# Performance work log

Hardware: AMD Instinct MI355X
Metric: run time of the kernel (lower is better)

## Reference

```python
import jax, jax.numpy as jnp
import numpy as np

LN_EPS = 1e-5   # torch nn.LayerNorm default eps
L2_EPS = 1e-12  # torch F.normalize default eps


def setup_inputs() -> dict:
    key = jax.random.key(0)
    k1, k2 = jax.random.split(key)
    b, c, h, w = 4, 256, 128, 256
    num_classes, num_prototype, proj_dim = 19, 10, 256
    x = jax.random.normal(k1, (b, c, h, w), dtype=jnp.float32)
    # trunc_normal_(std=0.02) approximated by normal * 0.02 (l2-normalized in fwd anyway)
    prototypes = jax.random.normal(k2, (num_classes, num_prototype, proj_dim), dtype=jnp.float32) * 0.02
    mask_norm_weight = jnp.ones((num_classes,), dtype=jnp.float32)
    mask_norm_bias = jnp.zeros((num_classes,), dtype=jnp.float32)
    return {"x": x, "prototypes": prototypes,
            "mask_norm_weight": mask_norm_weight, "mask_norm_bias": mask_norm_bias}


def _layer_norm(y, w, b):
    mu = jnp.mean(y, axis=-1, keepdims=True)
    var = jnp.var(y, axis=-1, keepdims=True)
    return (y - mu) * jax.lax.rsqrt(var + LN_EPS) * w + b


def reference(x, prototypes, mask_norm_weight, mask_norm_bias):
    b, c, h, w = x.shape
    # self.prototypes.data.copy_(l2_normalize(self.prototypes)) -- normalize over feature dim
    protos = prototypes / (jnp.linalg.norm(prototypes, axis=-1, keepdims=True) + L2_EPS)
    # rearrange 'b c h w -> (b h w) c'
    xf = x.transpose(0, 2, 3, 1).reshape(-1, c)           # [n, d]
    # cosine similarity: einsum('nd,kmd->nmk') then permute -> [n, k(classes), m(protos)]
    sim_mat = jnp.einsum('nd,kmd->nkm', xf, protos)       # [n, cls, proto]
    out_seg = jnp.max(sim_mat, axis=2)                    # amax over prototypes -> [n, cls]
    out_seg = _layer_norm(out_seg, mask_norm_weight, mask_norm_bias)
    # rearrange '(b h w) c -> b c h w'
    return out_seg.reshape(b, h, w, -1).transpose(0, 3, 1, 2)
```

## Files before the change

kernel.cpp:

```cpp
#include <hip/hip_runtime.h>


#define CC_   256
#define HW_   32768
#define NPIX_ 131072
#define NCLS_ 19
#define NPROT_ 10
#define NT_   12
#define MBLK_ 128
#define NCHUNK_ 8
#define ABUF_  16384
#define BBUF_  24576

typedef __attribute__((ext_vector_type(8))) short bf16x8;
typedef __attribute__((ext_vector_type(4))) float f32x4;

__device__ __forceinline__ void gll16(const void* g, void* l) {
  __builtin_amdgcn_global_load_lds((__attribute__((address_space(1))) void*)(g),
                                   (__attribute__((address_space(3))) void*)(l), 16, 0, 0);
}

__global__ void prep_protos(const float* __restrict__ protos, char* __restrict__ Bp) {
  const int p = blockIdx.x;
  const int l = threadIdx.x;
  __shared__ float pn[256];
  float v[4] = {0.f, 0.f, 0.f, 0.f};
  float sq = 0.f;
  if (p < 190) {
    #pragma unroll
    for (int i = 0; i < 4; ++i) {
      v[i] = protos[p * 256 + l * 4 + i];
      sq += v[i] * v[i];
    }
  }
  #pragma unroll
  for (int off = 32; off > 0; off >>= 1) sq += __shfl_xor(sq, off, 64);
  const float scale = (p < 190) ? 1.0f / (sqrtf(sq) + 1e-12f) : 0.0f;
  #pragma unroll
  for (int i = 0; i < 4; ++i) pn[l * 4 + i] = v[i] * scale;
  __syncthreads();

  const int oct  = l >> 1;
  const int part = l & 1;
  bf16x8 o8;
  #pragma unroll
  for (int i = 0; i < 8; ++i) {
    const float f = pn[oct * 8 + i];
    const unsigned bits = __builtin_bit_cast(unsigned, f);
    if (part == 0) {
      o8[i] = (short)(bits >> 16);
    } else {
      const float hf = __builtin_bit_cast(float, bits & 0xFFFF0000u);
      const float lf = f - hf;
      o8[i] = (short)(__builtin_bit_cast(unsigned, lf) >> 16);
    }
  }
  const int cc = oct >> 2, oL = oct & 3;
  const int nt = p >> 4;
  const int j2 = nt * 2 + part;
  const int lane = (oL << 4) | (p & 15);
  *(bf16x8*)(Bp + (size_t)(((cc * 24 + j2) * 64 + lane) * 16)) = o8;
}

__device__ __forceinline__ void convert_write(char* Adst, const float* xv,
                                              int chalf, int mt, int r15) {
  #pragma unroll
  for (int o2 = 0; o2 < 2; ++o2) {
    const int oct = chalf * 2 + o2;
    bf16x8 h, l;
    #pragma unroll
    for (int i = 0; i < 8; ++i) {
      const float f = xv[o2 * 8 + i];
      const unsigned bits = __builtin_bit_cast(unsigned, f);
      const float hf = __builtin_bit_cast(float, bits & 0xFFFF0000u);
      const float lf = f - hf;
      h[i] = (short)(bits >> 16);
      l[i] = (short)(__builtin_bit_cast(unsigned, lf) >> 16);
    }
    *(bf16x8*)(Adst + ((0 * 8 + mt) * 64 + (oct << 4) + r15) * 16) = h;
    *(bf16x8*)(Adst + ((1 * 8 + mt) * 64 + (oct << 4) + r15) * 16) = l;
  }
}

__launch_bounds__(256, 2)
__global__ void gemm_kernel(const float* __restrict__ x, const char* __restrict__ Bp,
                            const float* __restrict__ mw, const float* __restrict__ mb,
                            float* __restrict__ out) {
  __shared__ __align__(16) char smem[81920];
  char* Abase = smem;
  char* Bbase = smem + 32768;

  const int tid  = threadIdx.x;
  const int wave = tid >> 6;
  const int lane = tid & 63;
  const int n0   = blockIdx.x * MBLK_;
  const int b    = n0 >> 15;
  const int hw0  = n0 & (HW_ - 1);
  const float* xb = x + (size_t)b * CC_ * HW_ + hw0;

  const int pixl  = tid & 127;
  const int chalf = tid >> 7;
  const int mt_s  = pixl >> 4;
  const int r15   = pixl & 15;

  f32x4 acc[2][NT_];
  #pragma unroll
  for (int m = 0; m < 2; ++m)
    #pragma unroll
    for (int nt = 0; nt < NT_; ++nt) acc[m][nt] = (f32x4){0.f, 0.f, 0.f, 0.f};

  float xv[16];
  {
    const int c0 = chalf * 16;
    #pragma unroll
    for (int j = 0; j < 16; ++j) xv[j] = xb[(size_t)(c0 + j) * HW_ + pixl];
    #pragma unroll
    for (int i = 0; i < 6; ++i) {
      const int j2 = wave + 4 * i;
      gll16(Bp + (size_t)((j2 * 64 + lane) * 16), Bbase + j2 * 1024 + lane * 16);
    }
    convert_write(Abase, xv, chalf, mt_s, r15);
  }
  __syncthreads();

  int buf = 0;
  for (int cc = 0; cc < NCHUNK_; ++cc) {
    const int nb = buf ^ 1;
    if (cc + 1 < NCHUNK_) {
      const int c0 = (cc + 1) * 32 + chalf * 16;
      #pragma unroll
      for (int j = 0; j < 16; ++j) xv[j] = xb[(size_t)(c0 + j) * HW_ + pixl];
      #pragma unroll
      for (int i = 0; i < 6; ++i) {
        const int j2 = wave + 4 * i;
        gll16(Bp + (size_t)((((cc + 1) * 24 + j2) * 64 + lane) * 16),
              Bbase + nb * BBUF_ + j2 * 1024 + lane * 16);
      }
    }
    const char* A  = Abase + buf * ABUF_;
    const char* Bq = Bbase + buf * BBUF_;
    bf16x8 ahi[2], alo[2];
    #pragma unroll
    for (int m = 0; m < 2; ++m) {
      const int mt = wave * 2 + m;
      ahi[m] = *(const bf16x8*)(A + ((0 * 8 + mt) * 64 + lane) * 16);
      alo[m] = *(const bf16x8*)(A + ((1 * 8 + mt) * 64 + lane) * 16);
    }
    #pragma unroll
    for (int nt = 0; nt < NT_; ++nt) {
      const bf16x8 bhi = *(const bf16x8*)(Bq + ((nt * 2 + 0) * 64 + lane) * 16);
      const bf16x8 blo = *(const bf16x8*)(Bq + ((nt * 2 + 1) * 64 + lane) * 16);
      #pragma unroll
      for (int m = 0; m < 2; ++m) {
        acc[m][nt] = __builtin_amdgcn_mfma_f32_16x16x32_bf16(ahi[m], bhi, acc[m][nt], 0, 0, 0);
        acc[m][nt] = __builtin_amdgcn_mfma_f32_16x16x32_bf16(alo[m], bhi, acc[m][nt], 0, 0, 0);
        acc[m][nt] = __builtin_amdgcn_mfma_f32_16x16x32_bf16(ahi[m], blo, acc[m][nt], 0, 0, 0);
      }
    }
    if (cc + 1 < NCHUNK_) convert_write(Abase + nb * ABUF_, xv, chalf, mt_s, r15);
    __syncthreads();
    buf = nb;
  }

  float* sims = (float*)smem;
  for (int bat = 0; bat < 2; ++bat) {
    if ((wave >> 1) == bat) {
      const int wl = wave & 1;
      #pragma unroll
      for (int m = 0; m < 2; ++m) {
        const int pixbase = (wl * 2 + m) * 16 + (lane >> 4) * 4;
        #pragma unroll
        for (int nt = 0; nt < NT_; ++nt) {
          const int col = nt * 16 + (lane & 15);
          #pragma unroll
          for (int r = 0; r < 4; ++r)
            sims[(pixbase + r) * 193 + col] = acc[m][nt][r];
        }
      }
    }
    __syncthreads();
    if (tid < 64) {
      const int pl = bat * 64 + tid;
      float mx[NCLS_];
      #pragma unroll
      for (int k = 0; k < NCLS_; ++k) {
        float vmax = sims[tid * 193 + k * 10];
        #pragma unroll
        for (int m2 = 1; m2 < 10; ++m2)
          vmax = fmaxf(vmax, sims[tid * 193 + k * 10 + m2]);
        mx[k] = vmax;
      }
      float mu = 0.f;
      #pragma unroll
      for (int k = 0; k < NCLS_; ++k) mu += mx[k];
      mu *= (1.0f / NCLS_);
      float var = 0.f;
      #pragma unroll
      for (int k = 0; k < NCLS_; ++k) { const float d = mx[k] - mu; var += d * d; }
      var *= (1.0f / NCLS_);
      const float rstd = rsqrtf(var + 1e-5f);
      const int hw = hw0 + pl;
      #pragma unroll
      for (int k = 0; k < NCLS_; ++k) {
        out[((size_t)(b * NCLS_ + k) << 15) + hw] = (mx[k] - mu) * rstd * mw[k] + mb[k];
      }
    }
    __syncthreads();
  }
}

extern "C" void kernel_launch(void* const* d_in, const int* in_sizes, int n_in,
                              void* d_out, int out_size, void* d_ws, size_t ws_size,
                              hipStream_t stream) {
  const float* x      = (const float*)d_in[0];
  const float* protos = (const float*)d_in[1];
  const float* mw     = (const float*)d_in[2];
  const float* mb     = (const float*)d_in[3];
  float* out = (float*)d_out;
  char* Bp   = (char*)d_ws;

  prep_protos<<<192, 64, 0, stream>>>(protos, Bp);
  gemm_kernel<<<NPIX_ / MBLK_, 256, 0, stream>>>(x, Bp, mw, mb, out);
}
```

Before: 207.9 us.

## Switch to 32x32x16 MFMA with single-buffered LDS and register prefetch

Replaces the 16x16x32 bf16 MFMA tiling with 32x32x16 MFMA, where each wave owns a 32-pixel tile across all 192 prototype columns. A and B are now staged through registers into a single LDS buffer instead of double-buffered LDS filled by global_load_lds. This halves shared memory so that launch bounds can allow four blocks per CU. A wave now loads pairs of adjacent pixels with 8-byte loads, and the max reduction reads LDS with paired loads. The trade-off is an extra barrier per chunk and more register pressure from the prefetched loads, in exchange for higher occupancy and fewer MFMA issues.

```diff
diff --git a/kernel.cpp b/kernel.cpp
--- a/kernel.cpp
+++ b/kernel.cpp
@@ -5,20 +5,22 @@
 #define HW_   32768
 #define NPIX_ 131072
 #define NCLS_ 19
-#define NPROT_ 10
-#define NT_   12
 #define MBLK_ 128
-#define NCHUNK_ 8
-#define ABUF_  16384
-#define BBUF_  24576
-
-typedef __attribute__((ext_vector_type(8))) short bf16x8;
-typedef __attribute__((ext_vector_type(4))) float f32x4;
-
-__device__ __forceinline__ void gll16(const void* g, void* l) {
-  __builtin_amdgcn_global_load_lds((__attribute__((address_space(1))) void*)(g),
-                                   (__attribute__((address_space(3))) void*)(l), 16, 0, 0);
-}
+#define SIMST_ 194
+
+typedef __attribute__((ext_vector_type(8)))  short bf16x8;
+typedef __attribute__((ext_vector_type(16))) float f32x16;
+typedef __attribute__((ext_vector_type(4)))  float f32x4;
+typedef __attribute__((ext_vector_type(2)))  float f32x2;
+typedef __attribute__((ext_vector_type(4)))  unsigned int u32x4;
+
+#define RAWBAR() do {                                          \
+  __builtin_amdgcn_sched_barrier(0);                           \
+  asm volatile("s_waitcnt lgkmcnt(0)" ::: "memory");           \
+  __builtin_amdgcn_s_barrier();                                \
+  asm volatile("" ::: "memory");                               \
+  __builtin_amdgcn_sched_barrier(0);                           \
+} while (0)
 
 __global__ void prep_protos(const float* __restrict__ protos, char* __restrict__ Bp) {
   const int p = blockIdx.x;
@@ -42,53 +44,61 @@
 
   const int oct  = l >> 1;
   const int part = l & 1;
-  bf16x8 o8;
-  #pragma unroll
-  for (int i = 0; i < 8; ++i) {
-    const float f = pn[oct * 8 + i];
-    const unsigned bits = __builtin_bit_cast(unsigned, f);
+  unsigned int w[4];
+  #pragma unroll
+  for (int pr = 0; pr < 4; ++pr) {
+    const float f0 = pn[oct * 8 + 2 * pr];
+    const float f1 = pn[oct * 8 + 2 * pr + 1];
+    const unsigned int u0 = __builtin_bit_cast(unsigned int, f0);
+    const unsigned int u1 = __builtin_bit_cast(unsigned int, f1);
     if (part == 0) {
-      o8[i] = (short)(bits >> 16);
+      w[pr] = (u1 & 0xFFFF0000u) | (u0 >> 16);
     } else {
-      const float hf = __builtin_bit_cast(float, bits & 0xFFFF0000u);
-      const float lf = f - hf;
-      o8[i] = (short)(__builtin_bit_cast(unsigned, lf) >> 16);
-    }
-  }
-  const int cc = oct >> 2, oL = oct & 3;
-  const int nt = p >> 4;
-  const int j2 = nt * 2 + part;
-  const int lane = (oL << 4) | (p & 15);
-  *(bf16x8*)(Bp + (size_t)(((cc * 24 + j2) * 64 + lane) * 16)) = o8;
-}
-
-__device__ __forceinline__ void convert_write(char* Adst, const float* xv,
-                                              int chalf, int mt, int r15) {
-  #pragma unroll
-  for (int o2 = 0; o2 < 2; ++o2) {
-    const int oct = chalf * 2 + o2;
-    bf16x8 h, l;
+      const float t0 = __builtin_bit_cast(float, u0 & 0xFFFF0000u);
+      const float t1 = __builtin_bit_cast(float, u1 & 0xFFFF0000u);
+      const unsigned int v0 = __builtin_bit_cast(unsigned int, f0 - t0);
+      const unsigned int v1 = __builtin_bit_cast(unsigned int, f1 - t1);
+      w[pr] = (v1 & 0xFFFF0000u) | (v0 >> 16);
+    }
+  }
+  const int cc = oct >> 2, ks = (oct >> 1) & 1, ko = oct & 1;
+  const int nt = p >> 5, cL = p & 31;
+  const size_t a16 = (size_t)((((cc * 2 + ks) * 6 + nt) * 2 + part) * 64 + ko * 32 + cL);
+  *(u32x4*)(Bp + a16 * 16) = (u32x4){w[0], w[1], w[2], w[3]};
+}
+
+__device__ __forceinline__ void stageA(char* Albase, const f32x2* aLd,
+                                       int ksw, int kow, int mtw, int r15w) {
+  #pragma unroll
+  for (int e = 0; e < 2; ++e) {
+    unsigned int wh[4], wl[4];
     #pragma unroll
-    for (int i = 0; i < 8; ++i) {
-      const float f = xv[o2 * 8 + i];
-      const unsigned bits = __builtin_bit_cast(unsigned, f);
-      const float hf = __builtin_bit_cast(float, bits & 0xFFFF0000u);
-      const float lf = f - hf;
-      h[i] = (short)(bits >> 16);
-      l[i] = (short)(__builtin_bit_cast(unsigned, lf) >> 16);
-    }
-    *(bf16x8*)(Adst + ((0 * 8 + mt) * 64 + (oct << 4) + r15) * 16) = h;
-    *(bf16x8*)(Adst + ((1 * 8 + mt) * 64 + (oct << 4) + r15) * 16) = l;
-  }
-}
-
-__launch_bounds__(256, 2)
+    for (int pr = 0; pr < 4; ++pr) {
+      const float f0 = aLd[2 * pr][e];
+      const float f1 = aLd[2 * pr + 1][e];
+      const unsigned int u0 = __builtin_bit_cast(unsigned int, f0);
+      const unsigned int u1 = __builtin_bit_cast(unsigned int, f1);
+      wh[pr] = (u1 & 0xFFFF0000u) | (u0 >> 16);
+      const float t0 = __builtin_bit_cast(float, u0 & 0xFFFF0000u);
+      const float t1 = __builtin_bit_cast(float, u1 & 0xFFFF0000u);
+      const unsigned int v0 = __builtin_bit_cast(unsigned int, f0 - t0);
+      const unsigned int v1 = __builtin_bit_cast(unsigned int, f1 - t1);
+      wl[pr] = (v1 & 0xFFFF0000u) | (v0 >> 16);
+    }
+    char* bh = Albase + (size_t)((((ksw * 2 + 0) * 4 + mtw) * 64 + kow * 32 + e * 16 + r15w) * 16);
+    char* bl = Albase + (size_t)((((ksw * 2 + 1) * 4 + mtw) * 64 + kow * 32 + e * 16 + r15w) * 16);
+    *(u32x4*)bh = (u32x4){wh[0], wh[1], wh[2], wh[3]};
+    *(u32x4*)bl = (u32x4){wl[0], wl[1], wl[2], wl[3]};
+  }
+}
+
+__launch_bounds__(256, 4)
 __global__ void gemm_kernel(const float* __restrict__ x, const char* __restrict__ Bp,
                             const float* __restrict__ mw, const float* __restrict__ mb,
                             float* __restrict__ out) {
-  __shared__ __align__(16) char smem[81920];
-  char* Abase = smem;
-  char* Bbase = smem + 32768;
+  __shared__ __align__(16) char smem[40960];
+  char* Albase = smem;
+  char* Blbase = smem + 16384;
 
   const int tid  = threadIdx.x;
   const int wave = tid >> 6;
@@ -98,97 +108,86 @@
   const int hw0  = n0 & (HW_ - 1);
   const float* xb = x + (size_t)b * CC_ * HW_ + hw0;
 
-  const int pixl  = tid & 127;
-  const int chalf = tid >> 7;
-  const int mt_s  = pixl >> 4;
-  const int r15   = pixl & 15;
-
-  f32x4 acc[2][NT_];
-  #pragma unroll
-  for (int m = 0; m < 2; ++m)
+  const int oct  = wave;
+  const int ksw  = oct >> 1, kow = oct & 1;
+  const int mtw  = lane >> 4, r15w = lane & 15;
+  const float* xA = xb + (size_t)(oct * 8) * HW_ + 2 * lane;
+
+  f32x16 acc[6];
+  #pragma unroll
+  for (int nt = 0; nt < 6; ++nt) acc[nt] = (f32x16)(0.0f);
+
+  f32x2 aLd[8];
+  f32x4 bLd[6];
+
+  #pragma unroll
+  for (int j = 0; j < 8; ++j) aLd[j] = *(const f32x2*)(xA + (size_t)j * HW_);
+  #pragma unroll
+  for (int i = 0; i < 6; ++i) bLd[i] = *(const f32x4*)(Bp + (size_t)(tid + 256 * i) * 16);
+  stageA(Albase, aLd, ksw, kow, mtw, r15w);
+  #pragma unroll
+  for (int i = 0; i < 6; ++i) *(f32x4*)(Blbase + (size_t)(tid + 256 * i) * 16) = bLd[i];
+  __syncthreads();
+
+  #pragma unroll
+  for (int cc = 0; cc < 8; ++cc) {
+    if (cc < 7) {
+      const float* xAn = xA + (size_t)((cc + 1) * 32) * HW_;
+      #pragma unroll
+      for (int j = 0; j < 8; ++j) aLd[j] = *(const f32x2*)(xAn + (size_t)j * HW_);
+      #pragma unroll
+      for (int i = 0; i < 6; ++i)
+        bLd[i] = *(const f32x4*)(Bp + (size_t)(1536 * (cc + 1) + tid + 256 * i) * 16);
+    }
     #pragma unroll
-    for (int nt = 0; nt < NT_; ++nt) acc[m][nt] = (f32x4){0.f, 0.f, 0.f, 0.f};
-
-  float xv[16];
-  {
-    const int c0 = chalf * 16;
-    #pragma unroll
-    for (int j = 0; j < 16; ++j) xv[j] = xb[(size_t)(c0 + j) * HW_ + pixl];
-    #pragma unroll
-    for (int i = 0; i < 6; ++i) {
-      const int j2 = wave + 4 * i;
-      gll16(Bp + (size_t)((j2 * 64 + lane) * 16), Bbase + j2 * 1024 + lane * 16);
-    }
-    convert_write(Abase, xv, chalf, mt_s, r15);
-  }
-  __syncthreads();
-
-  int buf = 0;
-  for (int cc = 0; cc < NCHUNK_; ++cc) {
-    const int nb = buf ^ 1;
-    if (cc + 1 < NCHUNK_) {
-      const int c0 = (cc + 1) * 32 + chalf * 16;
-      #pragma unroll
-      for (int j = 0; j < 16; ++j) xv[j] = xb[(size_t)(c0 + j) * HW_ + pixl];
-      #pragma unroll
-      for (int i = 0; i < 6; ++i) {
-        const int j2 = wave + 4 * i;
-        gll16(Bp + (size_t)((((cc + 1) * 24 + j2) * 64 + lane) * 16),
-              Bbase + nb * BBUF_ + j2 * 1024 + lane * 16);
-      }
-    }
-    const char* A  = Abase + buf * ABUF_;
-    const char* Bq = Bbase + buf * BBUF_;
-    bf16x8 ahi[2], alo[2];
-    #pragma unroll
-    for (int m = 0; m < 2; ++m) {
-      const int mt = wave * 2 + m;
-      ahi[m] = *(const bf16x8*)(A + ((0 * 8 + mt) * 64 + lane) * 16);
-      alo[m] = *(const bf16x8*)(A + ((1 * 8 + mt) * 64 + lane) * 16);
-    }
-    #pragma unroll
-    for (int nt = 0; nt < NT_; ++nt) {
-      const bf16x8 bhi = *(const bf16x8*)(Bq + ((nt * 2 + 0) * 64 + lane) * 16);
-      const bf16x8 blo = *(const bf16x8*)(Bq + ((nt * 2 + 1) * 64 + lane) * 16);
-      #pragma unroll
-      for (int m = 0; m < 2; ++m) {
-        acc[m][nt] = __builtin_amdgcn_mfma_f32_16x16x32_bf16(ahi[m], bhi, acc[m][nt], 0, 0, 0);
-        acc[m][nt] = __builtin_amdgcn_mfma_f32_16x16x32_bf16(alo[m], bhi, acc[m][nt], 0, 0, 0);
-        acc[m][nt] = __builtin_amdgcn_mfma_f32_16x16x32_bf16(ahi[m], blo, acc[m][nt], 0, 0, 0);
-      }
-    }
-    if (cc + 1 < NCHUNK_) convert_write(Abase + nb * ABUF_, xv, chalf, mt_s, r15);
+    for (int ks = 0; ks < 2; ++ks) {
+      const bf16x8 ah = *(const bf16x8*)(Albase + (size_t)((((ks * 2 + 0) * 4 + wave) * 64 + lane) * 16));
+      const bf16x8 al = *(const bf16x8*)(Albase + (size_t)((((ks * 2 + 1) * 4 + wave) * 64 + lane) * 16));
+      #pragma unroll
+      for (int nt = 0; nt < 6; ++nt) {
+        const bf16x8 bh = *(const bf16x8*)(Blbase + (size_t)(((ks * 12 + nt * 2 + 0) * 64 + lane) * 16));
+        const bf16x8 bl = *(const bf16x8*)(Blbase + (size_t)(((ks * 12 + nt * 2 + 1) * 64 + lane) * 16));
+        acc[nt] = __builtin_amdgcn_mfma_f32_32x32x16_bf16(ah, bh, acc[nt], 0, 0, 0);
+        acc[nt] = __builtin_amdgcn_mfma_f32_32x32x16_bf16(al, bh, acc[nt], 0, 0, 0);
+        acc[nt] = __builtin_amdgcn_mfma_f32_32x32x16_bf16(ah, bl, acc[nt], 0, 0, 0);
+      }
+    }
+    RAWBAR();
+    if (cc < 7) {
+      stageA(Albase, aLd, ksw, kow, mtw, r15w);
+      #pragma unroll
+      for (int i = 0; i < 6; ++i) *(f32x4*)(Blbase + (size_t)(tid + 256 * i) * 16) = bLd[i];
+    }
     __syncthreads();
-    buf = nb;
   }
 
   float* sims = (float*)smem;
-  for (int bat = 0; bat < 2; ++bat) {
-    if ((wave >> 1) == bat) {
-      const int wl = wave & 1;
-      #pragma unroll
-      for (int m = 0; m < 2; ++m) {
-        const int pixbase = (wl * 2 + m) * 16 + (lane >> 4) * 4;
+  #pragma unroll 1
+  for (int r = 0; r < 4; ++r) {
+    if (wave == r) {
+      #pragma unroll
+      for (int nt = 0; nt < 6; ++nt) {
         #pragma unroll
-        for (int nt = 0; nt < NT_; ++nt) {
-          const int col = nt * 16 + (lane & 15);
-          #pragma unroll
-          for (int r = 0; r < 4; ++r)
-            sims[(pixbase + r) * 193 + col] = acc[m][nt][r];
+        for (int q = 0; q < 16; ++q) {
+          const int row = (q & 3) + 8 * (q >> 2) + 4 * (lane >> 5);
+          sims[row * SIMST_ + nt * 32 + (lane & 31)] = acc[nt][q];
         }
       }
     }
     __syncthreads();
-    if (tid < 64) {
-      const int pl = bat * 64 + tid;
+    if (tid < 32) {
       float mx[NCLS_];
       #pragma unroll
       for (int k = 0; k < NCLS_; ++k) {
-        float vmax = sims[tid * 193 + k * 10];
-        #pragma unroll
-        for (int m2 = 1; m2 < 10; ++m2)
-          vmax = fmaxf(vmax, sims[tid * 193 + k * 10 + m2]);
-        mx[k] = vmax;
+        const float* rp = sims + tid * SIMST_ + k * 10;
+        const f32x2 v0 = *(const f32x2*)(rp + 0);
+        const f32x2 v1 = *(const f32x2*)(rp + 2);
+        const f32x2 v2 = *(const f32x2*)(rp + 4);
+        const f32x2 v3 = *(const f32x2*)(rp + 6);
+        const f32x2 v4 = *(const f32x2*)(rp + 8);
+        float m01 = fmaxf(fmaxf(v0[0], v0[1]), fmaxf(v1[0], v1[1]));
+        float m23 = fmaxf(fmaxf(v2[0], v2[1]), fmaxf(v3[0], v3[1]));
+        mx[k] = fmaxf(fmaxf(m01, m23), fmaxf(v4[0], v4[1]));
       }
       float mu = 0.f;
       #pragma unroll
@@ -199,7 +198,7 @@
       for (int k = 0; k < NCLS_; ++k) { const float d = mx[k] - mu; var += d * d; }
       var *= (1.0f / NCLS_);
       const float rstd = rsqrtf(var + 1e-5f);
-      const int hw = hw0 + pl;
+      const int hw = hw0 + r * 32 + ((tid & 15) << 1) + ((tid >> 4) & 1);
       #pragma unroll
       for (int k = 0; k < NCLS_; ++k) {
         out[((size_t)(b * NCLS_ + k) << 15) + hw] = (mx[k] - mu) * rstd * mw[k] + mb[k];
```

After: 412.0 us. 98.2% more time.
